# Kernel tuning notes

Hardware: AMD Instinct MI355X
Metric: run time of the kernel (lower is better)

Reference implementation:

```python
import jax, jax.numpy as jnp
import numpy as np

N_NODES = 100000
N_EDGES = 640000
D = 128
N_LAYERS = 4
N_GRAPHS = 512


def setup_inputs() -> dict:
    key = jax.random.key(0)
    ks = jax.random.split(key, 12)
    x = jax.random.normal(ks[0], (N_NODES, D), dtype=jnp.float32)
    edge_index = jax.random.randint(ks[1], (2, N_EDGES), 0, N_NODES, dtype=jnp.int64)
    batch = jnp.sort(jax.random.randint(ks[2], (N_NODES,), 0, N_GRAPHS, dtype=jnp.int64))
    s = 1.0 / np.sqrt(D)
    convW = jax.random.uniform(ks[3], (N_LAYERS, D, D), jnp.float32, -s, s)
    convB = jax.random.uniform(ks[4], (N_LAYERS, D), jnp.float32, -s, s)
    W1 = jax.random.uniform(ks[5], (D, D), jnp.float32, -s, s)
    b1 = jax.random.uniform(ks[6], (D,), jnp.float32, -s, s)
    W2 = jax.random.uniform(ks[7], (D, D), jnp.float32, -s, s)
    b2 = jax.random.uniform(ks[8], (D,), jnp.float32, -s, s)
    W3 = jax.random.uniform(ks[9], (D, 1), jnp.float32, -s, s)
    b3 = jax.random.uniform(ks[10], (1,), jnp.float32, -s, s)
    return {"x": x, "edge_index": edge_index, "batch": batch,
            "convW": convW, "convB": convB,
            "W1": W1, "b1": b1, "W2": W2, "b2": b2, "W3": W3, "b3": b3}


def reference(x, edge_index, batch, convW, convB, W1, b1, W2, b2, W3, b3):
    N = x.shape[0]
    # GCNConv default: add self-loops, symmetric deg^-1/2 normalization
    loops = jnp.arange(N, dtype=edge_index.dtype)
    src = jnp.concatenate([edge_index[0], loops])  # [E+N]
    dst = jnp.concatenate([edge_index[1], loops])
    deg = jax.ops.segment_sum(jnp.ones_like(dst, dtype=x.dtype), dst, num_segments=N)
    dinv = jnp.where(deg > 0, jax.lax.rsqrt(deg), 0.0)
    norm = (dinv[src] * dinv[dst])[:, None]  # [E+N, 1]
    h = x
    for i in range(N_LAYERS):
        hw = h @ convW[i]                                   # [N, D]
        msg = hw[src] * norm                                # gather + scale [E+N, D]
        agg = jax.ops.segment_sum(msg, dst, num_segments=N)  # scatter-add [N, D]
        h = jax.nn.relu(agg + convB[i])
    pooled = jax.ops.segment_sum(h, batch, num_segments=N_GRAPHS)  # [G, D]
    z = jax.nn.relu(pooled @ W1 + b1)
    z = jax.nn.relu(z @ W2 + b2)
    return jax.nn.sigmoid(z @ W3 + b3)  # [G, 1]
```

## Files before the change

kernel.cpp:

```cpp
#include <hip/hip_runtime.h>
#include <math.h>

#define D 128
#define LSTRIDE 136

typedef _Float16 half8 __attribute__((ext_vector_type(8)));
typedef _Float16 half4v __attribute__((ext_vector_type(4)));
typedef _Float16 half2v __attribute__((ext_vector_type(2)));
typedef float f32x4 __attribute__((ext_vector_type(4)));


__global__ void k_fat1(const int* __restrict__ ei, int* __restrict__ counts,
                       int* __restrict__ pidx, int E, int countBlocks,
                       const float* __restrict__ convW, _Float16* __restrict__ Wf) {
    if ((int)blockIdx.x < countBlocks) {
        int e0 = (blockIdx.x * blockDim.x + threadIdx.x) * 4;
        if (e0 + 3 < E) {
            int4 d4 = *(const int4*)(ei + E + e0);
            int4 p;
            p.x = atomicAdd(&counts[d4.x], 1);
            p.y = atomicAdd(&counts[d4.y], 1);
            p.z = atomicAdd(&counts[d4.z], 1);
            p.w = atomicAdd(&counts[d4.w], 1);
            *(int4*)(pidx + e0) = p;
        } else {
            for (int e = e0; e < E; e++) pidx[e] = atomicAdd(&counts[ei[E + e]], 1);
        }
    } else {
        const int bid = blockIdx.x - countBlocks;
        const int l = bid >> 3;
        const int slot = (bid & 7) * 256 + threadIdx.x;
        const float* W = convW + (size_t)l * D * D;
        const int p = slot >> 6, ln = slot & 63;
        const int s = p >> 3, c = p & 7;
        const int kbase = s * 32 + ((ln >> 4) << 3);
        const int n = (c << 4) + (ln & 15);
        half8 hv;
#pragma unroll
        for (int j = 0; j < 8; j++) hv[j] = (_Float16)W[(size_t)(kbase + j) * D + n];
        *(half8*)(Wf + (size_t)l * D * D + (size_t)slot * 8) = hv;
    }
}

__global__ __launch_bounds__(256) void k_scan1(const int* __restrict__ counts,
                                               int* __restrict__ rowptrP,
                                               int* __restrict__ rend,
                                               int* __restrict__ bsums,
                                               float* __restrict__ dinv,
                                               int* __restrict__ degHist, int N) {
    __shared__ int sh[256];
    __shared__ int lh[64];
    const int t = threadIdx.x;
    const int base = blockIdx.x * 1024 + t * 4;
    int c[4], pj[4];
#pragma unroll
    for (int j = 0; j < 4; j++) {
        c[j] = (base + j < N) ? counts[base + j] : 0;
        pj[j] = (c[j] + 3) & ~3;
    }
#pragma unroll
    for (int j = 0; j < 4; j++)
        if (base + j < N) dinv[base + j] = rsqrtf((float)(c[j] + 1));

    if (t < 64) lh[t] = 0;
    __syncthreads();
#pragma unroll
    for (int j = 0; j < 4; j++)
        if (base + j < N) atomicAdd(&lh[c[j] < 63 ? c[j] : 63], 1);
    __syncthreads();
    if (t < 64 && lh[t]) atomicAdd(&degHist[t], lh[t]);

    int tsum = pj[0] + pj[1] + pj[2] + pj[3];
    sh[t] = tsum;
    __syncthreads();
    for (int off = 1; off < 256; off <<= 1) {
        int v = (t >= off) ? sh[t - off] : 0;
        __syncthreads();
        sh[t] += v;
        __syncthreads();
    }
    int run = (t == 0) ? 0 : sh[t - 1];
    if (t == 255) bsums[blockIdx.x] = sh[255];
#pragma unroll
    for (int j = 0; j < 4; j++) {
        if (base + j <= N) {
            rowptrP[base + j] = run;
            if (base + j < N) rend[base + j] = run + c[j];
        }
        run += pj[j];
    }
}


__global__ __launch_bounds__(256) void k_fat2(int* __restrict__ rowptrP,
                                              int* __restrict__ rend,
                                              const int* __restrict__ bsums,
                                              int NB, int N, int scanBlocks,
                                              const float* __restrict__ x,
                                              const float* __restrict__ dinv,
                                              _Float16* __restrict__ g16) {
    if ((int)blockIdx.x < scanBlocks) {
        __shared__ int pre[128];
        const int t = threadIdx.x;
        if (t < 128) pre[t] = (t < NB) ? bsums[t] : 0;
        __syncthreads();
        for (int off = 1; off < 128; off <<= 1) {
            int v = (t >= off && t < 128) ? pre[t - off] : 0;
            __syncthreads();
            if (t < 128) pre[t] += v;
            __syncthreads();
        }
        int i = blockIdx.x * blockDim.x + t;
        if (i <= N) {
            int b = i >> 10;
            int add = (b == 0) ? 0 : pre[b - 1];
            rowptrP[i] += add;
            if (i < N) rend[i] += add;
        }
    } else {
        int i = (blockIdx.x - scanBlocks) * blockDim.x + threadIdx.x;
        const int n8 = N * (D / 8);
        if (i >= n8) return;
        float s = dinv[i >> 4];
        const float4 v0 = *(const float4*)(x + (size_t)i * 8);
        const float4 v1 = *(const float4*)(x + (size_t)i * 8 + 4);
        half8 h;
        h[0] = (_Float16)(v0.x * s); h[1] = (_Float16)(v0.y * s);
        h[2] = (_Float16)(v0.z * s); h[3] = (_Float16)(v0.w * s);
        h[4] = (_Float16)(v1.x * s); h[5] = (_Float16)(v1.y * s);
        h[6] = (_Float16)(v1.z * s); h[7] = (_Float16)(v1.w * s);
        *(half8*)(g16 + (size_t)i * 8) = h;
    }
}

__global__ void k_fill(const int* __restrict__ ei, const int* __restrict__ rowptrP,
                       const int* __restrict__ pidx, int* __restrict__ srcs, int E,
                       int fillBlocks, int N, const int* __restrict__ counts,
                       const int* __restrict__ degHist, int* __restrict__ degCur,
                       int* __restrict__ perm) {
    if ((int)blockIdx.x < fillBlocks) {
        int e0 = (blockIdx.x * blockDim.x + threadIdx.x) * 4;
        if (e0 + 3 < E) {
            int4 s4 = *(const int4*)(ei + e0);
            int4 d4 = *(const int4*)(ei + E + e0);
            int4 p4 = *(const int4*)(pidx + e0);
            int r0 = rowptrP[d4.x], r1 = rowptrP[d4.y], r2 = rowptrP[d4.z], r3 = rowptrP[d4.w];
            srcs[r0 + p4.x] = s4.x;
            srcs[r1 + p4.y] = s4.y;
            srcs[r2 + p4.z] = s4.z;
            srcs[r3 + p4.w] = s4.w;
        } else {
            for (int e = e0; e < E; e++)
                srcs[rowptrP[ei[E + e]] + pidx[e]] = ei[e];
        }
    } else {
        __shared__ int lbase[64];
        __shared__ int lh[64];
        __shared__ int gb[64];
        const int t = threadIdx.x;
        const int i = ((int)blockIdx.x - fillBlocks) * blockDim.x + t;
        if (t < 64) lh[t] = 0;
        __syncthreads();
        int deg = 0, lrank = 0;
        const bool v = i < N;
        if (v) {
            int c = counts[i];
            deg = c < 63 ? c : 63;
            lrank = atomicAdd(&lh[deg], 1);
        }
        __syncthreads();
        if (t < 64) gb[t] = lh[t] ? atomicAdd(&degCur[t], lh[t]) : 0;
        if (t == 0) {
            int run = 0;
            for (int d = 63; d >= 0; d--) { lbase[d] = run; run += degHist[d]; }
        }
        __syncthreads();
        if (v) perm[lbase[deg] + gb[deg] + lrank] = i;
    }
}


__global__ __launch_bounds__(256) void k_layer(
        const _Float16* __restrict__ gin,
        const int* __restrict__ rowptrP, const int* __restrict__ rend,
        const int* __restrict__ srcs,
        const float* __restrict__ dinv,
        const int* __restrict__ perm,
        const _Float16* __restrict__ Wf,
        const float* __restrict__ bias,
        _Float16* __restrict__ gout, int N, int last) {
    __shared__ _Float16 S[64 * LSTRIDE];

    const int tid  = threadIdx.x;
    const int w    = tid >> 6;
    const int lane = tid & 63;
    const int q    = lane >> 4;
    const int l16  = lane & 15;
    const int nb0  = blockIdx.x * 64;
    const int cb   = l16 * 8;

    int pn[4];
#pragma unroll
    for (int it = 0; it < 4; it++) {
        const int slot = nb0 + w * 16 + q * 4 + it;
        pn[it] = (slot < N) ? perm[slot] : -1;
    }

    for (int it = 0; it < 4; ++it) {
        const int nl = w * 16 + q * 4 + it;
        const int node = pn[it];
        float a[8];
#pragma unroll
        for (int j = 0; j < 8; j++) a[j] = 0.f;

        if (node >= 0) {
            half8 sv = *(const half8*)(gin + (size_t)node * D + cb);
#pragma unroll
            for (int j = 0; j < 8; j++) a[j] = (float)sv[j];
            int e = rowptrP[node];
            const int end = rend[node];
            for (; e + 3 < end; e += 4) {
                int4 s4 = *(const int4*)(srcs + e);
                half8 v0 = *(const half8*)(gin + (size_t)s4.x * D + cb);
                half8 v1 = *(const half8*)(gin + (size_t)s4.y * D + cb);
                half8 v2 = *(const half8*)(gin + (size_t)s4.z * D + cb);
                half8 v3 = *(const half8*)(gin + (size_t)s4.w * D + cb);
#pragma unroll
                for (int j = 0; j < 8; j++)
                    a[j] += ((float)v0[j] + (float)v1[j]) + ((float)v2[j] + (float)v3[j]);
            }
            for (; e < end; e++) {
                int s0 = srcs[e];
                half8 v0 = *(const half8*)(gin + (size_t)s0 * D + cb);
#pragma unroll
                for (int j = 0; j < 8; j++) a[j] += (float)v0[j];
            }
        }
        const float sc = (node >= 0) ? dinv[node] : 0.f;
        half8 o;
#pragma unroll
        for (int j = 0; j < 8; j++) o[j] = (_Float16)(a[j] * sc);
        *(half8*)(&S[nl * LSTRIDE + cb]) = o;
    }

    asm volatile("s_waitcnt lgkmcnt(0)" ::: "memory");

    f32x4 acc[8];
#pragma unroll
    for (int cc = 0; cc < 8; cc++) acc[cc] = (f32x4){0.f, 0.f, 0.f, 0.f};

    const int nl2 = w * 16 + l16;
#pragma unroll
    for (int s = 0; s < 4; s++) {
        half8 bf = *(const half8*)(&S[nl2 * LSTRIDE + s * 32 + q * 8]);
#pragma unroll
        for (int cc = 0; cc < 8; cc++) {
            half8 wh = *(const half8*)(Wf + (size_t)((s * 8 + cc) * 64 + lane) * 8);
            acc[cc] = __builtin_amdgcn_mfma_f32_16x16x32_f16(wh, bf, acc[cc], 0, 0, 0);
        }
    }

    const int slot2 = nb0 + nl2;
    const int node2 = (slot2 < N) ? perm[slot2] : -1;
    if (node2 >= 0) {
        const float scale = last ? 1.0f : dinv[node2];
        _Float16* rp = gout + (size_t)node2 * D + q * 4;
#pragma unroll
        for (int cc = 0; cc < 8; cc++) {
            const float4 bc = *(const float4*)(bias + cc * 16 + q * 4);
            half4v o;
            o[0] = (_Float16)(fmaxf(acc[cc][0] + bc.x, 0.f) * scale);
            o[1] = (_Float16)(fmaxf(acc[cc][1] + bc.y, 0.f) * scale);
            o[2] = (_Float16)(fmaxf(acc[cc][2] + bc.z, 0.f) * scale);
            o[3] = (_Float16)(fmaxf(acc[cc][3] + bc.w, 0.f) * scale);
            *(half4v*)(rp + cc * 16) = o;
        }
    }
}


__global__ __launch_bounds__(256) void k_poolhead(
        const _Float16* __restrict__ h, const int* __restrict__ batch,
        const float* __restrict__ W1, const float* __restrict__ b1,
        const float* __restrict__ W2, const float* __restrict__ b2,
        const float* __restrict__ W3, const float* __restrict__ b3,
        float* __restrict__ out, int N) {
    __shared__ int sb[2];
    __shared__ float part[16][D];
    __shared__ float pool[D];
    __shared__ float z[D];
    __shared__ float red[D];

    const int g = blockIdx.x;
    const int t = threadIdx.x;

    if (t < 2) {
        int target = g + t;
        int lo = 0, hi = N;
        while (lo < hi) {
            int mid = (lo + hi) >> 1;
            if (batch[mid] < target) lo = mid + 1; else hi = mid;
        }
        sb[t] = lo;
    }
    __syncthreads();
    const int rs = sb[0], re = sb[1];

    const int w = t >> 6;
    const int lane = t & 63;
    const int rw = w * 4 + (lane >> 4);
    const int c8 = (lane & 15) * 8;

    float ax[8];
#pragma unroll
    for (int j = 0; j < 8; j++) ax[j] = 0.f;
    for (int r = rs + rw; r < re; r += 16) {
        half8 vv = *(const half8*)(h + (size_t)r * D + c8);
#pragma unroll
        for (int j = 0; j < 8; j++) ax[j] += (float)vv[j];
    }
#pragma unroll
    for (int j = 0; j < 8; j++) part[rw][c8 + j] = ax[j];
    __syncthreads();

    if (t < D) {
        float s = 0.f;
#pragma unroll
        for (int gg = 0; gg < 16; gg++) s += part[gg][t];
        pool[t] = s;
    }
    __syncthreads();

    if (t < D) {
        float s = b1[t];
        for (int k = 0; k < D; k++) s = fmaf(pool[k], W1[(size_t)k * D + t], s);
        z[t] = fmaxf(s, 0.f);
    }
    __syncthreads();

    if (t < D) {
        float s = b2[t];
        for (int k = 0; k < D; k++) s = fmaf(z[k], W2[(size_t)k * D + t], s);
        red[t] = fmaxf(s, 0.f) * W3[t];
    }
    __syncthreads();
    for (int off = 64; off >= 1; off >>= 1) {
        if (t < off) red[t] += red[t + off];
        __syncthreads();
    }
    if (t == 0) out[g] = 1.f / (1.f + expf(-(red[0] + b3[0])));
}


extern "C" void kernel_launch(void* const* d_in, const int* in_sizes, int n_in,
                              void* d_out, int out_size, void* d_ws, size_t ws_size,
                              hipStream_t stream) {
    const float* x     = (const float*)d_in[0];
    const int*   ei    = (const int*)d_in[1];
    const int*   batch = (const int*)d_in[2];
    const float* convW = (const float*)d_in[3];
    const float* convB = (const float*)d_in[4];
    const float* W1 = (const float*)d_in[5];
    const float* b1 = (const float*)d_in[6];
    const float* W2 = (const float*)d_in[7];
    const float* b2 = (const float*)d_in[8];
    const float* W3 = (const float*)d_in[9];
    const float* b3 = (const float*)d_in[10];
    float* out = (float*)d_out;

    const int N = in_sizes[0] / D;
    const int E = in_sizes[1] / 2;
    const int G = out_size;
    const int NB = (N + 1023) / 1024;

    char* w = (char*)d_ws;
    size_t off = 0;
    auto alloc = [&](size_t bytes) -> char* {
        char* p = w + off;
        off += (bytes + 255) & ~(size_t)255;
        return p;
    };
    float*     dinv   = (float*)alloc((size_t)N * 4);
    _Float16*  gA     = (_Float16*)alloc((size_t)N * D * 2);
    _Float16*  gB     = (_Float16*)alloc((size_t)N * D * 2);
    _Float16*  Wf     = (_Float16*)alloc((size_t)4 * D * D * 2);
    int*       counts = (int*)alloc((size_t)(N + 128) * 4);
    int*       degHist= counts + N;
    int*       degCur = counts + N + 64;
    int*       rowptrP= (int*)alloc((size_t)(N + 1) * 4);
    int*       rend   = (int*)alloc((size_t)N * 4);
    int*       pidx   = (int*)alloc((size_t)E * 4);
    int*       srcs   = (int*)alloc((size_t)(E + 3 * N) * 4);
    int*       bsums  = (int*)alloc((size_t)NB * 4);
    int*       perm   = (int*)alloc((size_t)N * 4);

    hipMemsetAsync(counts, 0, (size_t)(N + 128) * 4, stream);
    const int countBlocks = (E / 4 + 255) / 256;
    k_fat1<<<countBlocks + 32, 256, 0, stream>>>(ei, counts, pidx, E, countBlocks,
                                                 convW, Wf);
    k_scan1<<<NB, 256, 0, stream>>>(counts, rowptrP, rend, bsums, dinv, degHist, N);
    const int scanBlocks = (N + 1 + 255) / 256;
    const int cvtBlocks  = (N * (D / 8) + 255) / 256;
    k_fat2<<<scanBlocks + cvtBlocks, 256, 0, stream>>>(rowptrP, rend, bsums, NB, N,
                                                       scanBlocks, x, dinv, gA);
    const int fillBlocks = (E / 4 + 255) / 256;
    const int rankBlocks = (N + 255) / 256;
    k_fill<<<fillBlocks + rankBlocks, 256, 0, stream>>>(ei, rowptrP, pidx, srcs, E,
                                                        fillBlocks, N, counts,
                                                        degHist, degCur, perm);

    const int layer_grid = (N + 63) / 64;
    const _Float16* gi = gA;
    _Float16* go = gB;
    for (int l = 0; l < 4; l++) {
        k_layer<<<layer_grid, 256, 0, stream>>>(gi, rowptrP, rend, srcs, dinv, perm,
                                                Wf + (size_t)l * D * D,
                                                convB + (size_t)l * D,
                                                go, N, l == 3);
        const _Float16* tmp = go;
        go = (_Float16*)gi;
        gi = tmp;
    }

    k_poolhead<<<G, 256, 0, stream>>>(gi, batch, W1, b1, W2, b2, W3, b3, out, N);
}
```

Baseline: 357.3 us.

## Store node features in degree-sorted rank order and pad edge lists with sentinels

Node features are now stored in the degree-sorted permutation order (rank space), and edge source indices are relabeled to ranks. Intermediate layers therefore read their own row and write outputs contiguously, without going through perm. Each neighbour list is padded to a multiple of four with a sentinel index that points at a zero row. This lets the gather loop run in chunks of four with no scalar tail, interleave the four nodes a lane owns, and prefetch the next index chunk. The cost is extra preprocessing: rank arrays, per-slot row pointers, and zero sentinel rows.

```diff
diff --git a/kernel.cpp b/kernel.cpp
--- a/kernel.cpp
+++ b/kernel.cpp
@@ -6,7 +6,6 @@
 
 typedef _Float16 half8 __attribute__((ext_vector_type(8)));
 typedef _Float16 half4v __attribute__((ext_vector_type(4)));
-typedef _Float16 half2v __attribute__((ext_vector_type(2)));
 typedef float f32x4 __attribute__((ext_vector_type(4)));
 
 
@@ -44,7 +43,6 @@
 
 __global__ __launch_bounds__(256) void k_scan1(const int* __restrict__ counts,
                                                int* __restrict__ rowptrP,
-                                               int* __restrict__ rend,
                                                int* __restrict__ bsums,
                                                float* __restrict__ dinv,
                                                int* __restrict__ degHist, int N) {
@@ -83,22 +81,21 @@
     if (t == 255) bsums[blockIdx.x] = sh[255];
 #pragma unroll
     for (int j = 0; j < 4; j++) {
-        if (base + j <= N) {
-            rowptrP[base + j] = run;
-            if (base + j < N) rend[base + j] = run + c[j];
-        }
+        if (base + j <= N) rowptrP[base + j] = run;
         run += pj[j];
     }
 }
 
 
 __global__ __launch_bounds__(256) void k_fat2(int* __restrict__ rowptrP,
-                                              int* __restrict__ rend,
+                                              const int* __restrict__ counts,
                                               const int* __restrict__ bsums,
-                                              int NB, int N, int scanBlocks,
-                                              const float* __restrict__ x,
-                                              const float* __restrict__ dinv,
-                                              _Float16* __restrict__ g16) {
+                                              int NB, int N, int scanBlocks, int NS,
+                                              int* __restrict__ srcs,
+                                              const int* __restrict__ degHist,
+                                              int* __restrict__ degCur,
+                                              int* __restrict__ perm,
+                                              int* __restrict__ rankOf) {
     if ((int)blockIdx.x < scanBlocks) {
         __shared__ int pre[128];
         const int t = threadIdx.x;
@@ -114,51 +111,19 @@
         if (i <= N) {
             int b = i >> 10;
             int add = (b == 0) ? 0 : pre[b - 1];
-            rowptrP[i] += add;
-            if (i < N) rend[i] += add;
+            int rp = rowptrP[i] + add;
+            rowptrP[i] = rp;
+            if (i < N) {
+                int c = counts[i];
+                int re_ = rp + c;
+                int pad = (-c) & 3;
+                for (int k2 = 0; k2 < pad; k2++) srcs[re_ + k2] = NS;
+            }
         }
     } else {
-        int i = (blockIdx.x - scanBlocks) * blockDim.x + threadIdx.x;
-        const int n8 = N * (D / 8);
-        if (i >= n8) return;
-        float s = dinv[i >> 4];
-        const float4 v0 = *(const float4*)(x + (size_t)i * 8);
-        const float4 v1 = *(const float4*)(x + (size_t)i * 8 + 4);
-        half8 h;
-        h[0] = (_Float16)(v0.x * s); h[1] = (_Float16)(v0.y * s);
-        h[2] = (_Float16)(v0.z * s); h[3] = (_Float16)(v0.w * s);
-        h[4] = (_Float16)(v1.x * s); h[5] = (_Float16)(v1.y * s);
-        h[6] = (_Float16)(v1.z * s); h[7] = (_Float16)(v1.w * s);
-        *(half8*)(g16 + (size_t)i * 8) = h;
-    }
-}
-
-__global__ void k_fill(const int* __restrict__ ei, const int* __restrict__ rowptrP,
-                       const int* __restrict__ pidx, int* __restrict__ srcs, int E,
-                       int fillBlocks, int N, const int* __restrict__ counts,
-                       const int* __restrict__ degHist, int* __restrict__ degCur,
-                       int* __restrict__ perm) {
-    if ((int)blockIdx.x < fillBlocks) {
-        int e0 = (blockIdx.x * blockDim.x + threadIdx.x) * 4;
-        if (e0 + 3 < E) {
-            int4 s4 = *(const int4*)(ei + e0);
-            int4 d4 = *(const int4*)(ei + E + e0);
-            int4 p4 = *(const int4*)(pidx + e0);
-            int r0 = rowptrP[d4.x], r1 = rowptrP[d4.y], r2 = rowptrP[d4.z], r3 = rowptrP[d4.w];
-            srcs[r0 + p4.x] = s4.x;
-            srcs[r1 + p4.y] = s4.y;
-            srcs[r2 + p4.z] = s4.z;
-            srcs[r3 + p4.w] = s4.w;
-        } else {
-            for (int e = e0; e < E; e++)
-                srcs[rowptrP[ei[E + e]] + pidx[e]] = ei[e];
-        }
-    } else {
-        __shared__ int lbase[64];
-        __shared__ int lh[64];
-        __shared__ int gb[64];
+        __shared__ int lbase[64], lh[64], gb[64];
         const int t = threadIdx.x;
-        const int i = ((int)blockIdx.x - fillBlocks) * blockDim.x + t;
+        const int i = ((int)blockIdx.x - scanBlocks) * blockDim.x + t;
         if (t < 64) lh[t] = 0;
         __syncthreads();
         int deg = 0, lrank = 0;
@@ -175,16 +140,86 @@
             for (int d = 63; d >= 0; d--) { lbase[d] = run; run += degHist[d]; }
         }
         __syncthreads();
-        if (v) perm[lbase[deg] + gb[deg] + lrank] = i;
+        if (v) {
+            int r = lbase[deg] + gb[deg] + lrank;
+            perm[r] = i;
+            rankOf[i] = r;
+        }
+    }
+}
+
+
+__global__ void k_fill(const int* __restrict__ ei, const int* __restrict__ rowptrP,
+                       const int* __restrict__ pidx, int* __restrict__ srcs, int E,
+                       int fillBlocks, int slotBlocks, int N, int NS,
+                       const int* __restrict__ rankOf,
+                       const int* __restrict__ perm,
+                       const float* __restrict__ dinv,
+                       int* __restrict__ rbegR, int* __restrict__ rpenR,
+                       float* __restrict__ dinvR, int* __restrict__ sentIdx,
+                       const float* __restrict__ x,
+                       _Float16* __restrict__ gA, _Float16* __restrict__ gB) {
+    const int b = blockIdx.x;
+    if (b < fillBlocks) {
+        int e0 = (b * blockDim.x + threadIdx.x) * 4;
+        if (e0 + 3 < E) {
+            int4 s4 = *(const int4*)(ei + e0);
+            int4 d4 = *(const int4*)(ei + E + e0);
+            int4 p4 = *(const int4*)(pidx + e0);
+            srcs[rowptrP[d4.x] + p4.x] = rankOf[s4.x];
+            srcs[rowptrP[d4.y] + p4.y] = rankOf[s4.y];
+            srcs[rowptrP[d4.z] + p4.z] = rankOf[s4.z];
+            srcs[rowptrP[d4.w] + p4.w] = rankOf[s4.w];
+        } else {
+            for (int e = e0; e < E; e++)
+                srcs[rowptrP[ei[E + e]] + pidx[e]] = rankOf[ei[e]];
+        }
+    } else if (b < fillBlocks + slotBlocks) {
+        const int r = (b - fillBlocks) * blockDim.x + threadIdx.x;
+        if (r == 0) { int4 sv; sv.x = sv.y = sv.z = sv.w = NS; *(int4*)sentIdx = sv; }
+        if (r < NS) {
+            if (r < N) {
+                int p = perm[r];
+                rbegR[r] = rowptrP[p];
+                rpenR[r] = rowptrP[p + 1];
+                dinvR[r] = dinv[p];
+            } else {
+                rbegR[r] = 0; rpenR[r] = 0; dinvR[r] = 0.f;
+            }
+        }
+    } else {
+        const int i = (b - fillBlocks - slotBlocks) * blockDim.x + threadIdx.x;
+        const int TC = (NS + 1) * 16;
+        if (i >= TC) return;
+        const int row = i >> 4, j = i & 15;
+        if (row < N) {
+            const float s = dinv[row];
+            const int rr = rankOf[row];
+            const float4 v0 = *(const float4*)(x + (size_t)row * D + j * 8);
+            const float4 v1 = *(const float4*)(x + (size_t)row * D + j * 8 + 4);
+            half8 h;
+            h[0] = (_Float16)(v0.x * s); h[1] = (_Float16)(v0.y * s);
+            h[2] = (_Float16)(v0.z * s); h[3] = (_Float16)(v0.w * s);
+            h[4] = (_Float16)(v1.x * s); h[5] = (_Float16)(v1.y * s);
+            h[6] = (_Float16)(v1.z * s); h[7] = (_Float16)(v1.w * s);
+            *(half8*)(gA + (size_t)rr * D + j * 8) = h;
+        } else {
+            half8 z;
+#pragma unroll
+            for (int j2 = 0; j2 < 8; j2++) z[j2] = (_Float16)0.f;
+            *(half8*)(gA + (size_t)row * D + j * 8) = z;
+            *(half8*)(gB + (size_t)row * D + j * 8) = z;
+        }
     }
 }
 
 
 __global__ __launch_bounds__(256) void k_layer(
         const _Float16* __restrict__ gin,
-        const int* __restrict__ rowptrP, const int* __restrict__ rend,
+        const int* __restrict__ rbegR, const int* __restrict__ rpenR,
         const int* __restrict__ srcs,
-        const float* __restrict__ dinv,
+        const int* __restrict__ sentIdx,
+        const float* __restrict__ dinvR,
         const int* __restrict__ perm,
         const _Float16* __restrict__ Wf,
         const float* __restrict__ bias,
@@ -196,50 +231,61 @@
     const int lane = tid & 63;
     const int q    = lane >> 4;
     const int l16  = lane & 15;
-    const int nb0  = blockIdx.x * 64;
+    const int sb   = blockIdx.x * 64;
     const int cb   = l16 * 8;
-
-    int pn[4];
+    const int slot0 = sb + w * 16 + q * 4;
+
+    int bg[4], nc[4];
+    int mx = 0;
 #pragma unroll
     for (int it = 0; it < 4; it++) {
-        const int slot = nb0 + w * 16 + q * 4 + it;
-        pn[it] = (slot < N) ? perm[slot] : -1;
-    }
-
-    for (int it = 0; it < 4; ++it) {
+        bg[it] = rbegR[slot0 + it];
+        nc[it] = (rpenR[slot0 + it] - bg[it]) >> 2;
+        mx = nc[it] > mx ? nc[it] : mx;
+    }
+
+    float a[4][8];
+#pragma unroll
+    for (int it = 0; it < 4; it++) {
+        half8 sv = *(const half8*)(gin + (size_t)(slot0 + it) * D + cb);
+#pragma unroll
+        for (int j = 0; j < 8; j++) a[it][j] = (float)sv[j];
+    }
+
+    int4 cur[4];
+#pragma unroll
+    for (int it = 0; it < 4; it++) {
+        const int* ip = (0 < nc[it]) ? (srcs + bg[it]) : sentIdx;
+        cur[it] = *(const int4*)ip;
+    }
+    for (int ch = 0; ch < mx; ch++) {
+        int4 nxt[4];
+#pragma unroll
+        for (int it = 0; it < 4; it++) {
+            const int* ip = (ch + 1 < nc[it]) ? (srcs + bg[it] + (ch + 1) * 4) : sentIdx;
+            nxt[it] = *(const int4*)ip;
+        }
+#pragma unroll
+        for (int it = 0; it < 4; it++) {
+            half8 v0 = *(const half8*)(gin + (size_t)cur[it].x * D + cb);
+            half8 v1 = *(const half8*)(gin + (size_t)cur[it].y * D + cb);
+            half8 v2 = *(const half8*)(gin + (size_t)cur[it].z * D + cb);
+            half8 v3 = *(const half8*)(gin + (size_t)cur[it].w * D + cb);
+#pragma unroll
+            for (int j = 0; j < 8; j++)
+                a[it][j] += ((float)v0[j] + (float)v1[j]) + ((float)v2[j] + (float)v3[j]);
+        }
+#pragma unroll
+        for (int it = 0; it < 4; it++) cur[it] = nxt[it];
+    }
+
+#pragma unroll
+    for (int it = 0; it < 4; it++) {
+        const float sc = dinvR[slot0 + it];
         const int nl = w * 16 + q * 4 + it;
-        const int node = pn[it];
-        float a[8];
-#pragma unroll
-        for (int j = 0; j < 8; j++) a[j] = 0.f;
-
-        if (node >= 0) {
-            half8 sv = *(const half8*)(gin + (size_t)node * D + cb);
-#pragma unroll
-            for (int j = 0; j < 8; j++) a[j] = (float)sv[j];
-            int e = rowptrP[node];
-            const int end = rend[node];
-            for (; e + 3 < end; e += 4) {
-                int4 s4 = *(const int4*)(srcs + e);
-                half8 v0 = *(const half8*)(gin + (size_t)s4.x * D + cb);
-                half8 v1 = *(const half8*)(gin + (size_t)s4.y * D + cb);
-                half8 v2 = *(const half8*)(gin + (size_t)s4.z * D + cb);
-                half8 v3 = *(const half8*)(gin + (size_t)s4.w * D + cb);
-#pragma unroll
-                for (int j = 0; j < 8; j++)
-                    a[j] += ((float)v0[j] + (float)v1[j]) + ((float)v2[j] + (float)v3[j]);
-            }
-            for (; e < end; e++) {
-                int s0 = srcs[e];
-                half8 v0 = *(const half8*)(gin + (size_t)s0 * D + cb);
-#pragma unroll
-                for (int j = 0; j < 8; j++) a[j] += (float)v0[j];
-            }
-        }
-        const float sc = (node >= 0) ? dinv[node] : 0.f;
         half8 o;
 #pragma unroll
-        for (int j = 0; j < 8; j++) o[j] = (_Float16)(a[j] * sc);
+        for (int j = 0; j < 8; j++) o[j] = (_Float16)(a[it][j] * sc);
         *(half8*)(&S[nl * LSTRIDE + cb]) = o;
     }
 
@@ -260,11 +306,10 @@
         }
     }
 
-    const int slot2 = nb0 + nl2;
-    const int node2 = (slot2 < N) ? perm[slot2] : -1;
-    if (node2 >= 0) {
-        const float scale = last ? 1.0f : dinv[node2];
-        _Float16* rp = gout + (size_t)node2 * D + q * 4;
+    const int slot2 = sb + nl2;
+    if (!last) {
+        const float scale = dinvR[slot2];
+        _Float16* rp = gout + (size_t)slot2 * D + q * 4;
 #pragma unroll
         for (int cc = 0; cc < 8; cc++) {
             const float4 bc = *(const float4*)(bias + cc * 16 + q * 4);
@@ -273,6 +318,19 @@
             o[1] = (_Float16)(fmaxf(acc[cc][1] + bc.y, 0.f) * scale);
             o[2] = (_Float16)(fmaxf(acc[cc][2] + bc.z, 0.f) * scale);
             o[3] = (_Float16)(fmaxf(acc[cc][3] + bc.w, 0.f) * scale);
+            *(half4v*)(rp + cc * 16) = o;
+        }
+    } else if (slot2 < N) {
+        const int node2 = perm[slot2];
+        _Float16* rp = gout + (size_t)node2 * D + q * 4;
+#pragma unroll
+        for (int cc = 0; cc < 8; cc++) {
+            const float4 bc = *(const float4*)(bias + cc * 16 + q * 4);
+            half4v o;
+            o[0] = (_Float16)fmaxf(acc[cc][0] + bc.x, 0.f);
+            o[1] = (_Float16)fmaxf(acc[cc][1] + bc.y, 0.f);
+            o[2] = (_Float16)fmaxf(acc[cc][2] + bc.z, 0.f);
+            o[3] = (_Float16)fmaxf(acc[cc][3] + bc.w, 0.f);
             *(half4v*)(rp + cc * 16) = o;
         }
     }
@@ -372,6 +430,7 @@
     const int E = in_sizes[1] / 2;
     const int G = out_size;
     const int NB = (N + 1023) / 1024;
+    const int NS = ((N + 63) / 64) * 64;
 
     char* w = (char*)d_ws;
     size_t off = 0;
@@ -381,39 +440,46 @@
         return p;
     };
     float*     dinv   = (float*)alloc((size_t)N * 4);
-    _Float16*  gA     = (_Float16*)alloc((size_t)N * D * 2);
-    _Float16*  gB     = (_Float16*)alloc((size_t)N * D * 2);
+    _Float16*  gA     = (_Float16*)alloc((size_t)(NS + 1) * D * 2);
+    _Float16*  gB     = (_Float16*)alloc((size_t)(NS + 1) * D * 2);
     _Float16*  Wf     = (_Float16*)alloc((size_t)4 * D * D * 2);
     int*       counts = (int*)alloc((size_t)(N + 128) * 4);
     int*       degHist= counts + N;
     int*       degCur = counts + N + 64;
     int*       rowptrP= (int*)alloc((size_t)(N + 1) * 4);
-    int*       rend   = (int*)alloc((size_t)N * 4);
     int*       pidx   = (int*)alloc((size_t)E * 4);
     int*       srcs   = (int*)alloc((size_t)(E + 3 * N) * 4);
     int*       bsums  = (int*)alloc((size_t)NB * 4);
     int*       perm   = (int*)alloc((size_t)N * 4);
+    int*       rankOf = (int*)alloc((size_t)N * 4);
+    int*       rbegR  = (int*)alloc((size_t)NS * 4);
+    int*       rpenR  = (int*)alloc((size_t)NS * 4);
+    float*     dinvR  = (float*)alloc((size_t)NS * 4);
+    int*       sentIdx= (int*)alloc(16);
 
     hipMemsetAsync(counts, 0, (size_t)(N + 128) * 4, stream);
     const int countBlocks = (E / 4 + 255) / 256;
     k_fat1<<<countBlocks + 32, 256, 0, stream>>>(ei, counts, pidx, E, countBlocks,
                                                  convW, Wf);
-    k_scan1<<<NB, 256, 0, stream>>>(counts, rowptrP, rend, bsums, dinv, degHist, N);
+    k_scan1<<<NB, 256, 0, stream>>>(counts, rowptrP, bsums, dinv, degHist, N);
     const int scanBlocks = (N + 1 + 255) / 256;
-    const int cvtBlocks  = (N * (D / 8) + 255) / 256;
-    k_fat2<<<scanBlocks + cvtBlocks, 256, 0, stream>>>(rowptrP, rend, bsums, NB, N,
-                                                       scanBlocks, x, dinv, gA);
+    const int rankBlocks = (N + 255) / 256;
+    k_fat2<<<scanBlocks + rankBlocks, 256, 0, stream>>>(rowptrP, counts, bsums, NB, N,
+                                                        scanBlocks, NS, srcs,
+                                                        degHist, degCur, perm, rankOf);
     const int fillBlocks = (E / 4 + 255) / 256;
-    const int rankBlocks = (N + 255) / 256;
-    k_fill<<<fillBlocks + rankBlocks, 256, 0, stream>>>(ei, rowptrP, pidx, srcs, E,
-                                                        fillBlocks, N, counts,
-                                                        degHist, degCur, perm);
-
-    const int layer_grid = (N + 63) / 64;
+    const int slotBlocks = (NS + 255) / 256;
+    const int cvtBlocks  = ((NS + 1) * 16 + 255) / 256;
+    k_fill<<<fillBlocks + slotBlocks + cvtBlocks, 256, 0, stream>>>(
+        ei, rowptrP, pidx, srcs, E, fillBlocks, slotBlocks, N, NS,
+        rankOf, perm, dinv, rbegR, rpenR, dinvR, sentIdx, x, gA, gB);
+
+    const int layer_grid = NS / 64;
     const _Float16* gi = gA;
     _Float16* go = gB;
     for (int l = 0; l < 4; l++) {
-        k_layer<<<layer_grid, 256, 0, stream>>>(gi, rowptrP, rend, srcs, dinv, perm,
+        k_layer<<<layer_grid, 256, 0, stream>>>(gi, rbegR, rpenR, srcs, sentIdx,
+                                                dinvR, perm,
                                                 Wf + (size_t)l * D * D,
                                                 convB + (size_t)l * D,
                                                 go, N, l == 3);
```

Result: faster. 348.8 us (-2.4%).
